# Performance work log

Hardware: AMD Instinct MI355X
Metric: run time of the kernel (lower is better)

## Reference

```python
import jax, jax.numpy as jnp
import numpy as np

H = 128  # GRU hidden size


def _conv(x, w, b, stride):
    # x: NCHW, w: OIHW, VALID padding (torch Conv2d default padding=0)
    y = jax.lax.conv_general_dilated(x, w, (stride, stride), 'VALID',
                                     dimension_numbers=('NCHW', 'OIHW', 'NCHW'))
    return y + b[None, :, None, None]


def setup_inputs() -> dict:
    key = jax.random.key(0)
    ks = jax.random.split(key, 16)
    T, B, A = 128, 32, 6
    x = jax.random.uniform(ks[0], (T * B, 1, 84, 84), jnp.float32) * 255.0
    done = (jax.random.uniform(ks[1], (T * B,)) < 0.1).astype(jnp.float32)
    gru_state = jnp.zeros((1, B, H), jnp.float32)
    s = 0.05
    params = dict(
        conv1_w=jax.random.normal(ks[2], (32, 1, 8, 8)) * s,
        conv1_b=jnp.zeros((32,)),
        conv2_w=jax.random.normal(ks[3], (64, 32, 4, 4)) * s,
        conv2_b=jnp.zeros((64,)),
        conv3_w=jax.random.normal(ks[4], (64, 64, 3, 3)) * s,
        conv3_b=jnp.zeros((64,)),
        fc_w=jax.random.normal(ks[5], (512, 64 * 7 * 7)) * 0.02,
        fc_b=jnp.zeros((512,)),
        w_ih=jax.random.normal(ks[6], (3 * H, 512)) * 0.04,
        w_hh=jax.random.normal(ks[7], (3 * H, H)) * 0.08,
        b_ih=jnp.zeros((3 * H,)),
        b_hh=jnp.zeros((3 * H,)),
        actor_w=jax.random.normal(ks[8], (A, H)) * 0.01,
        actor_b=jnp.zeros((A,)),
        critic_w=jax.random.normal(ks[9], (1, H)) * 0.09,
        critic_b=jnp.zeros((1,)),
    )
    return dict(x=x, done=done, gru_state=gru_state, **params)


def reference(x, done, gru_state,
              conv1_w, conv1_b, conv2_w, conv2_b, conv3_w, conv3_b,
              fc_w, fc_b, w_ih, w_hh, b_ih, b_hh,
              actor_w, actor_b, critic_w, critic_b):
    # CNN encoder on x/255
    h = jax.nn.relu(_conv(x / 255.0, conv1_w, conv1_b, 4))  # [N,32,20,20]
    h = jax.nn.relu(_conv(h, conv2_w, conv2_b, 2))          # [N,64,9,9]
    h = jax.nn.relu(_conv(h, conv3_w, conv3_b, 1))          # [N,64,7,7]
    feat = jax.nn.relu(h.reshape(h.shape[0], -1) @ fc_w.T + fc_b)  # [N,512]

    B = gru_state.shape[1]
    feat = feat.reshape(-1, B, feat.shape[-1])  # [T,B,512]
    d = done.reshape(-1, B)                     # [T,B]

    # hoist input-to-gate projection out of the scan
    gx = jnp.einsum('tbi,gi->tbg', feat, w_ih) + b_ih  # [T,B,3H]

    def step(hprev, inp):
        gxt, dt = inp
        hprev = (1.0 - dt)[:, None] * hprev  # done-reset mask
        gh = hprev @ w_hh.T + b_hh           # [B,3H]
        r = jax.nn.sigmoid(gxt[:, :H] + gh[:, :H])
        z = jax.nn.sigmoid(gxt[:, H:2 * H] + gh[:, H:2 * H])
        n = jnp.tanh(gxt[:, 2 * H:] + r * gh[:, 2 * H:])
        hnew = (1.0 - z) * n + z * hprev
        return hnew, hnew

    h_final, hs = jax.lax.scan(step, gru_state[0], (gx, d))
    hidden = hs.reshape(-1, H)  # [T*B,H]

    logits = hidden @ actor_w.T + actor_b   # [N,A]
    value = hidden @ critic_w.T + critic_b  # [N,1]
    return logits, value, h_final[None]
```

## Files before the change

kernel.cpp:

```cpp
#include <hip/hip_runtime.h>
#include <hip/hip_bf16.h>
#include <stdint.h>

#define DI __device__ __forceinline__

typedef __bf16 bf16x8 __attribute__((ext_vector_type(8)));
typedef __bf16 bf16x4 __attribute__((ext_vector_type(4)));
typedef float f32x16 __attribute__((ext_vector_type(16)));
typedef float f32x2 __attribute__((ext_vector_type(2)));

DI float bf2f(unsigned short u){ return __uint_as_float(((unsigned int)u)<<16); }
DI unsigned short f2bf(float f){
  unsigned int x = __float_as_uint(f);
  x += 0x7fffu + ((x>>16)&1u);
  return (unsigned short)(x>>16);
}
DI float sigmoidf_(float x){ return 1.0f/(1.0f + __expf(-x)); }
DI float tanhf_(float x){ return 2.0f/(1.0f + __expf(-2.0f*x)) - 1.0f; }

DI void gld_lds16(const void* g, void* l){
  __builtin_amdgcn_global_load_lds((const __attribute__((address_space(1))) void*)g,
                                   (__attribute__((address_space(3))) void*)l, 16, 0, 0);
}
DI f32x16 mfma32(bf16x8 a, bf16x8 b, f32x16 c){
  return __builtin_amdgcn_mfma_f32_32x32x16_bf16(a, b, c, 0, 0, 0);
}

__global__ __launch_bounds__(256) void k_prep_all(
    const float* __restrict__ w1, const float* __restrict__ w2, const float* __restrict__ w3,
    const float* __restrict__ fcw, const float* __restrict__ wih,
    unsigned short* __restrict__ W1P, unsigned short* __restrict__ W2P,
    unsigned short* __restrict__ W3P, unsigned short* __restrict__ FCWP,
    unsigned short* __restrict__ GXWP)
{
  const int blk = blockIdx.x, tid = threadIdx.x;
  if (blk < 8){
    int idx = blk*256 + tid;
    int j=idx&7, l=(idx>>3)&63, kk=idx>>9;
    int oc=l&31, kg=kk*16+((l>>5)<<3)+j;
    W1P[idx] = f2bf(w1[oc*64 + kg] * (1.0f/255.0f));
  } else if (blk < 136){
    int idx = (blk-8)*256 + tid;
    int j=idx&7, l=(idx>>3)&63, nt=(idx>>9)&1, kh=(idx>>10)&1, s=idx>>11;
    int oc=nt*32+(l&31), ic=kh*16+(l>>5)*8+j, ky=s>>2, kx=s&3;
    W2P[idx] = f2bf(w2[((oc*32+ic)*4+ky)*4+kx]);
  } else if (blk < 280){
    int idx = (blk-136)*256 + tid;
    int j=idx&7, l=(idx>>3)&63, nt=(idx>>9)&1, kh=(idx>>10)&3, s=idx>>12;
    int oc=nt*32+(l&31), ic=kh*16+(l>>5)*8+j, ky=s/3, kx=s-ky*3;
    W3P[idx] = f2bf(w3[((oc*64+ic)*3+ky)*3+kx]);
  } else if (blk < 6552){
    int i = (blk-280)*256 + tid;
    int t2 = i&511, rest = i>>9;
    int ks = rest%196, nt = rest/196;
    int j=t2&7, l=t2>>3;
    int n=nt*32+(l&31), k=ks*16+(l>>5)*8+j;
    int c=k&63, pos=k>>6;
    float wv = fcw[(size_t)n*3136 + c*49 + pos];
    unsigned short hi = f2bf(wv);
    FCWP[i] = hi;
    FCWP[1605632 + i] = f2bf(wv - bf2f(hi));
  } else {
    int i = (blk-6552)*256 + tid;
    int t2 = i&511, rest = i>>9;
    int ks = rest&31, nt = rest>>5;
    int j=t2&7, l=t2>>3;
    int n=nt*32+(l&31), k=ks*16+(l>>5)*8+j;
    float wv = wih[(size_t)n*512 + k];
    unsigned short hi = f2bf(wv);
    GXWP[i] = hi;
    GXWP[196608 + i] = f2bf(wv - bf2f(hi));
  }
}

__global__ __launch_bounds__(256) void k_conv1(const float* __restrict__ x,
    const unsigned short* __restrict__ w1p, const float* __restrict__ b,
    unsigned short* __restrict__ a1, int nbase)
{
  __shared__ __align__(16) char imgs[4*14784];
  const int tid=threadIdx.x, l=tid&63, w=tid>>6;
  const int nloc = blockIdx.x*4 + w;
  char* myimg = imgs + w*14784;
  const float* xp = x + (size_t)(nbase+nloc)*7056;

  for (int it=0; it<28; ++it){
    int idx4 = l + it*64;
    if (idx4 < 1764){
      float4 v = *(const float4*)(xp + idx4*4);
      int row = idx4/21, rem = idx4 - row*21;
      ushort4 u; u.x=f2bf(v.x); u.y=f2bf(v.y); u.z=f2bf(v.z); u.w=f2bf(v.w);
      *(ushort4*)(myimg + row*176 + rem*8) = u;
    }
  }

  bf16x8 wb[4];
  #pragma unroll
  for (int kk=0;kk<4;kk++) wb[kk] = *(const bf16x8*)(w1p + (kk*64 + l)*8);
  const float bias = b[l&31];
  asm volatile("s_waitcnt lgkmcnt(0)" ::: "memory");

  const int kyh = (l>>5);
  unsigned short* obase = a1 + (size_t)nloc*12800;
  for (int mt=0; mt<13; ++mt){
    int p = mt*32 + (l&31);
    p = min(p, 399);
    const int oy = p/20, ox = p - oy*20;
    const int rbyte = oy*4*176 + ox*8;
    f32x16 acc = {};
    #pragma unroll
    for (int kk=0;kk<4;kk++){
      const int a = rbyte + (kk*2 + kyh)*176;
      bf16x8 af;
      *(bf16x4*)&af       = *(const bf16x4*)(myimg + a);
      *((bf16x4*)&af + 1) = *(const bf16x4*)(myimg + a + 8);
      acc = mfma32(af, wb[kk], acc);
    }
    const int oc = l&31;
    #pragma unroll
    for (int rg=0;rg<16;rg++){
      int row = (rg&3) + 8*(rg>>2) + 4*kyh;
      int pos = mt*32 + row;
      if (pos < 400)
        obase[pos*32 + oc] = f2bf(fmaxf(acc[rg] + bias, 0.f));
    }
  }
}

__global__ __launch_bounds__(256) void k_conv2(const unsigned short* __restrict__ a1,
    const unsigned short* __restrict__ w2p, const float* __restrict__ b2,
    unsigned short* __restrict__ a2, int nbase)
{
  extern __shared__ __align__(16) char smem[];
  const int tid=threadIdx.x, l=tid&63, w=tid>>6;
  const int nloc = blockIdx.x*4 + w;
  char* myimg = smem + w*25600;
  const char* gimg = (const char*)(a1 + (size_t)nloc*12800);
  #pragma unroll
  for (int i=0;i<25;i++){
    int o = i*1024 + l*16;
    int q = o ^ (((o>>7)&7)<<4);
    gld_lds16(gimg + q, myimg + i*1024);
  }
  __syncthreads();
  int rbase[3];
  #pragma unroll
  for (int mt=0;mt<3;mt++){
    int r = mt*32 + (l&31);
    int oy=r/9, ox=r-oy*9;
    rbase[mt] = 40*oy + 2*ox;
  }
  const int grp16 = (l>>5)*16;
  f32x16 acc[3][2] = {};
  #pragma unroll
  for (int ky=0;ky<4;ky++){
    #pragma unroll
    for (int kx=0;kx<4;kx++){
      const int s = ky*4+kx;
      #pragma unroll
      for (int kh=0;kh<2;kh++){
        bf16x8 b0 = *(const bf16x8*)(w2p + (((s*2+kh)*2+0)*64 + l)*8);
        bf16x8 b1 = *(const bf16x8*)(w2p + (((s*2+kh)*2+1)*64 + l)*8);
        #pragma unroll
        for (int mt=0;mt<3;mt++){
          int ip = rbase[mt] + ky*20 + kx;
          ip = min(ip, 399);
          int byte = (ip*64 + kh*32 + grp16) ^ (((ip>>1)&7)<<4);
          bf16x8 af = *(const bf16x8*)(myimg + byte);
          acc[mt][0] = mfma32(af, b0, acc[mt][0]);
          acc[mt][1] = mfma32(af, b1, acc[mt][1]);
        }
      }
    }
  }
  const float bias0 = b2[l&31], bias1 = b2[32+(l&31)];
  unsigned short* ob = (unsigned short*)myimg;
  #pragma unroll
  for (int mt=0;mt<3;mt++){
    #pragma unroll
    for (int rg=0;rg<16;rg++){
      int r = mt*32 + (rg&3) + 8*(rg>>2) + 4*(l>>5);
      ob[r*64 + (l&31)]      = f2bf(fmaxf(acc[mt][0][rg]+bias0,0.f));
      ob[r*64 + 32 + (l&31)] = f2bf(fmaxf(acc[mt][1][rg]+bias1,0.f));
    }
  }
  asm volatile("s_waitcnt lgkmcnt(0)" ::: "memory");
  const uint4* s4 = (const uint4*)ob;
  uint4* d4 = (uint4*)(a2 + (size_t)(nbase+nloc)*5184);
  #pragma unroll
  for (int i=0;i<11;i++){
    int c = i*64 + l;
    if (c < 648) d4[c] = s4[c];
  }
}

__global__ __launch_bounds__(256) void k_conv3(const unsigned short* __restrict__ a2,
    const unsigned short* __restrict__ w3p, const float* __restrict__ b3,
    unsigned short* __restrict__ a3)
{
  __shared__ __align__(16) char smem3[4*11264];
  const int tid=threadIdx.x, l=tid&63, w=tid>>6;
  const int n = blockIdx.x*4 + w;
  char* myimg = smem3 + w*11264;
  const char* gimg = (const char*)(a2 + (size_t)n*5184);
  #pragma unroll
  for (int i=0;i<11;i++){
    int c = i*64 + l;
    int cc = min(c, 647);
    int o = cc*16;
    int q = o ^ (((o>>7)&7)<<4);
    gld_lds16(gimg + q, myimg + i*1024);
  }
  __syncthreads();
  int base[2];
  #pragma unroll
  for (int mt=0;mt<2;mt++){
    int r = mt*32 + (l&31);
    int oy=r/7, ox=r-oy*7;
    base[mt] = oy*9 + ox;
  }
  const int grp16 = (l>>5)*16;
  f32x16 acc[2][2] = {};
  #pragma unroll
  for (int ky=0;ky<3;ky++){
    #pragma unroll
    for (int kx=0;kx<3;kx++){
      const int s = ky*3+kx;
      #pragma unroll
      for (int kh=0;kh<4;kh++){
        bf16x8 b0 = *(const bf16x8*)(w3p + (((s*4+kh)*2+0)*64 + l)*8);
        bf16x8 b1 = *(const bf16x8*)(w3p + (((s*4+kh)*2+1)*64 + l)*8);
        #pragma unroll
        for (int mt=0;mt<2;mt++){
          int ip = min(base[mt] + ky*9 + kx, 80);
          int byte = (ip*128 + kh*32 + grp16) ^ ((ip&7)<<4);
          bf16x8 af = *(const bf16x8*)(myimg + byte);
          acc[mt][0] = mfma32(af, b0, acc[mt][0]);
          acc[mt][1] = mfma32(af, b1, acc[mt][1]);
        }
      }
    }
  }
  const float bias0 = b3[l&31], bias1 = b3[32+(l&31)];
  unsigned short* ob = (unsigned short*)myimg;
  #pragma unroll
  for (int mt=0;mt<2;mt++){
    #pragma unroll
    for (int rg=0;rg<16;rg++){
      int r = mt*32 + (rg&3) + 8*(rg>>2) + 4*(l>>5);
      if (r < 49){
        ob[r*64 + (l&31)]      = f2bf(fmaxf(acc[mt][0][rg]+bias0,0.f));
        ob[r*64 + 32 + (l&31)] = f2bf(fmaxf(acc[mt][1][rg]+bias1,0.f));
      }
    }
  }
  asm volatile("s_waitcnt lgkmcnt(0)" ::: "memory");
  const uint4* s4 = (const uint4*)ob;
  uint4* d4 = (uint4*)(a3 + (size_t)n*3136);
  #pragma unroll
  for (int i=0;i<7;i++){
    int c = i*64 + l;
    if (c < 392) d4[c] = s4[c];
  }
}

template<bool RELU, bool OBF16, bool HILO>
__global__ __launch_bounds__(256) void k_gemm(const unsigned short* __restrict__ A, int K,
    const unsigned short* __restrict__ Wp, int loOff, const float* __restrict__ bias,
    void* __restrict__ out, int N)
{
  __shared__ __align__(16) char ab[2][8192];
  const int tid=threadIdx.x, l=tid&63, w=tid>>6;
  const int m0=blockIdx.y*128, n0=blockIdx.x*64;
  const int KS=K>>4, T=K>>5;
  const int mh=w&1, ntl=w>>1;
  const int ntg = blockIdx.x*2 + ntl;
  const char* Ab = (const char*)A;

  f32x16 acc[2] = {};
  bf16x8 bh0, bh1, bl0, bl1, nh0, nh1, nl0, nl1;

  #pragma unroll
  for (int i=0;i<2;i++){
    int o = (w*2+i)*1024 + l*16;
    int q = o ^ (((o>>7)&7)<<4);
    int row = q>>6, kc=(q>>4)&3;
    gld_lds16(Ab + ((size_t)(m0+row)*K)*2 + kc*16, ab[0] + (w*2+i)*1024);
  }
  {
    const unsigned short* p0 = Wp + ((size_t)(ntg*KS)*64 + l)*8;
    bh0 = *(const bf16x8*)(p0);
    bh1 = *(const bf16x8*)(p0 + 512);
    if (HILO){
      bl0 = *(const bf16x8*)(p0 + loOff);
      bl1 = *(const bf16x8*)(p0 + loOff + 512);
    }
  }
  __syncthreads();

  for (int t=0;t<T;t++){
    const int cb = t&1;
    if (t+1 < T){
      #pragma unroll
      for (int i=0;i<2;i++){
        int o = (w*2+i)*1024 + l*16;
        int q = o ^ (((o>>7)&7)<<4);
        int row = q>>6, kc=(q>>4)&3;
        gld_lds16(Ab + ((size_t)(m0+row)*K + (t+1)*32)*2 + kc*16, ab[cb^1] + (w*2+i)*1024);
      }
      const unsigned short* pn = Wp + ((size_t)(ntg*KS + (t+1)*2)*64 + l)*8;
      nh0 = *(const bf16x8*)(pn);
      nh1 = *(const bf16x8*)(pn + 512);
      if (HILO){
        nl0 = *(const bf16x8*)(pn + loOff);
        nl1 = *(const bf16x8*)(pn + loOff + 512);
      }
    }
    #pragma unroll
    for (int mt=0;mt<2;mt++){
      int r = mh*64 + mt*32 + (l&31);
      int b0 = (r*64 + (l>>5)*16) ^ (((r>>1)&7)<<4);
      bf16x8 a0 = *(const bf16x8*)(ab[cb] + b0);
      bf16x8 a1 = *(const bf16x8*)(ab[cb] + (b0^32));
      acc[mt] = mfma32(a0, bh0, acc[mt]);
      acc[mt] = mfma32(a1, bh1, acc[mt]);
      if (HILO){
        acc[mt] = mfma32(a0, bl0, acc[mt]);
        acc[mt] = mfma32(a1, bl1, acc[mt]);
      }
    }
    __syncthreads();
    bh0=nh0; bh1=nh1;
    if (HILO){ bl0=nl0; bl1=nl1; }
  }

  const int col = n0 + ntl*32 + (l&31);
  const float bv = bias[col];
  #pragma unroll
  for (int mt=0;mt<2;mt++){
    #pragma unroll
    for (int rg=0;rg<16;rg++){
      int r = m0 + mh*64 + mt*32 + (rg&3) + 8*(rg>>2) + 4*(l>>5);
      float v = acc[mt][rg] + bv;
      if (RELU) v = fmaxf(v, 0.f);
      if (OBF16) ((unsigned short*)out)[(size_t)r*N + col] = f2bf(v);
      else       ((float*)out)[(size_t)r*N + col] = v;
    }
  }
}

__global__ __launch_bounds__(256) void k_gru(const float* __restrict__ gx,
    const float* __restrict__ done, const float* __restrict__ h0,
    const float* __restrict__ whh, const float* __restrict__ bhh,
    float* __restrict__ hid, float* __restrict__ hfin)
{
  __shared__ __align__(16) float hs[2][128];
  const int b = blockIdx.x, tid = threadIdx.x;
  const int u = tid>>1, sub = tid&1;
  f32x2 wr[32], wz[32], wn[32];
  const float* wru = whh + (size_t)u*128 + sub*64;
  const float* wzu = whh + (size_t)(u+128)*128 + sub*64;
  const float* wnu = whh + (size_t)(u+256)*128 + sub*64;
  #pragma unroll
  for (int q=0;q<16;q++){
    const int e = (q + sub*4)&15;
    float4 a = *(const float4*)(wru + e*4);
    float4 c = *(const float4*)(wzu + e*4);
    float4 d = *(const float4*)(wnu + e*4);
    wr[q*2] = f32x2{a.x,a.y}; wr[q*2+1] = f32x2{a.z,a.w};
    wz[q*2] = f32x2{c.x,c.y}; wz[q*2+1] = f32x2{c.z,c.w};
    wn[q*2] = f32x2{d.x,d.y}; wn[q*2+1] = f32x2{d.z,d.w};
  }
  const float br = bhh[u], bz = bhh[u+128], bn = bhh[u+256];
  if (tid<128) hs[0][tid] = h0[(size_t)b*128+tid];

  const float* g0 = gx + (size_t)b*384;
  float pg0 = g0[u], pg1 = g0[u+128], pg2 = g0[u+256];
  float pd  = done[b];
  __syncthreads();

  for (int t=0;t<128;t++){
    const int cur = t&1;
    const float gr=pg0, gz=pg1, gn=pg2, dn=pd;
    if (t+1 < 128){
      const float* gp = gx + ((size_t)(t+1)*32+b)*384;
      pg0=gp[u]; pg1=gp[u+128]; pg2=gp[u+256];
      pd = done[(t+1)*32+b];
    }
    const float hpv = hs[cur][u];
    const float* hb = &hs[cur][sub*64];
    f32x2 hv[32];
    #pragma unroll
    for (int q=0;q<16;q++){
      const int e = (q + sub*4)&15;
      float4 v = *(const float4*)(hb + e*4);
      hv[q*2]   = f32x2{v.x,v.y};
      hv[q*2+1] = f32x2{v.z,v.w};
    }
    f32x2 a2r = {0.f,0.f}, a2z = {0.f,0.f}, a2n = {0.f,0.f};
    #pragma unroll
    for (int i=0;i<32;i++){
      a2r += wr[i]*hv[i];
      a2z += wz[i]*hv[i];
      a2n += wn[i]*hv[i];
    }
    float ar=a2r[0]+a2r[1], az=a2z[0]+a2z[1], an=a2n[0]+a2n[1];
    ar += __shfl_xor(ar,1);
    az += __shfl_xor(az,1);
    an += __shfl_xor(an,1);
    if (sub==0){
      const float keep = 1.0f - dn;
      const float hp = keep*hpv;
      const float r  = sigmoidf_(gr + keep*ar + br);
      const float z  = sigmoidf_(gz + keep*az + bz);
      const float nn = tanhf_  (gn + r*(keep*an + bn));
      const float hn = (1.0f-z)*nn + z*hp;
      hs[cur^1][u] = hn;
      hid[((size_t)t*32+b)*128 + u] = hn;
    }
    asm volatile("s_waitcnt lgkmcnt(0)\n\ts_barrier" ::: "memory");
    __builtin_amdgcn_sched_barrier(0);
  }
  if (tid<128) hfin[(size_t)b*128+tid] = hs[0][tid];
}

__global__ __launch_bounds__(256) void k_heads(const float* __restrict__ hid,
    const float* __restrict__ aw, const float* __restrict__ ab,
    const float* __restrict__ cw, const float* __restrict__ cb,
    float* __restrict__ out)
{
  __shared__ __align__(16) float wsm[7*128];
  __shared__ float bb[7];
  const int tid = threadIdx.x;
  for (int i=tid;i<896;i+=256) wsm[i] = (i<768) ? aw[i] : cw[i-768];
  if (tid<7) bb[tid] = (tid<6) ? ab[tid] : cb[0];
  __syncthreads();
  const int idx = blockIdx.x*256 + tid;
  const int n = idx/7, a = idx - n*7;
  const float4* hp = (const float4*)(hid + (size_t)n*128);
  const float4* wp = (const float4*)(&wsm[a*128]);
  float s = bb[a];
  #pragma unroll
  for (int q=0;q<32;q++){
    const float4 h4=hp[q], w4=wp[q];
    s += h4.x*w4.x + h4.y*w4.y + h4.z*w4.z + h4.w*w4.w;
  }
  if (a<6) out[(size_t)n*6+a]=s; else out[24576+n]=s;
}

extern "C" void kernel_launch(void* const* d_in, const int* in_sizes, int n_in,
                              void* d_out, int out_size, void* d_ws, size_t ws_size,
                              hipStream_t stream)
{
  const float* x    = (const float*)d_in[0];
  const float* done = (const float*)d_in[1];
  const float* h0   = (const float*)d_in[2];
  const float* c1w  = (const float*)d_in[3];
  const float* c1b  = (const float*)d_in[4];
  const float* c2w  = (const float*)d_in[5];
  const float* c2b  = (const float*)d_in[6];
  const float* c3w  = (const float*)d_in[7];
  const float* c3b  = (const float*)d_in[8];
  const float* fcw  = (const float*)d_in[9];
  const float* fcb  = (const float*)d_in[10];
  const float* wih  = (const float*)d_in[11];
  const float* whh  = (const float*)d_in[12];
  const float* bih  = (const float*)d_in[13];
  const float* bhh  = (const float*)d_in[14];
  const float* aw   = (const float*)d_in[15];
  const float* ab   = (const float*)d_in[16];
  const float* cw   = (const float*)d_in[17];
  const float* cb   = (const float*)d_in[18];
  float* out = (float*)d_out;
  char* ws = (char*)d_ws;

  unsigned short* W1P  = (unsigned short*)(ws);
  unsigned short* W2P  = (unsigned short*)(ws + 4096);
  unsigned short* W3P  = (unsigned short*)(ws + 69632);
  unsigned short* FCWP = (unsigned short*)(ws + 143360);
  unsigned short* GXWP = (unsigned short*)(ws + 6565888);
  unsigned short* A1   = (unsigned short*)(ws + 7352320);
  unsigned short* A2   = (unsigned short*)(ws + 59781120);
  unsigned short* A3   = (unsigned short*)(ws + 7352320);
  unsigned short* FEAT = (unsigned short*)(ws + 33042432);
  float* GX   = (float*)(ws + 37236736);
  float* HID  = (float*)(ws + 43528192);

  static bool attr_set = false;
  if (!attr_set) {
    (void)hipFuncSetAttribute((const void*)k_conv2, hipFuncAttributeMaxDynamicSharedMemorySize, 102400);
    attr_set = true;
  }

  k_prep_all<<<7320, 256, 0, stream>>>(c1w, c2w, c3w, fcw, wih, W1P, W2P, W3P, FCWP, GXWP);

  for (int pass=0; pass<2; pass++){
    k_conv1<<<512, 256, 0, stream>>>(x, W1P, c1b, A1, pass*2048);
    k_conv2<<<512, 256, 102400, stream>>>(A1, W2P, c2b, A2, pass*2048);
  }
  k_conv3<<<1024, 256, 0, stream>>>(A2, W3P, c3b, A3);
  k_gemm<true, true, false><<<dim3(8,32), 256, 0, stream>>>(A3, 3136, FCWP, 0, fcb, (void*)FEAT, 512);
  k_gemm<false,false,true ><<<dim3(6,32), 256, 0, stream>>>(FEAT, 512, GXWP, 196608, bih, (void*)GX, 384);
  k_gru<<<32, 256, 0, stream>>>(GX, done, h0, whh, bhh, HID, out + 28672);
  k_heads<<<112, 256, 0, stream>>>(HID, aw, ab, cw, cb, out);
}
```

Measured before the change: 342.2 us.

## Run GRU recurrence as single-block bf16 MFMA over all batch columns

Replaces the per-batch-row scalar GRU kernel (32 blocks of FMA dot products) with one 512-thread block that computes the hidden-to-gate product for all 32 batch rows per step using 16x16x32 bf16 MFMA, with W_hh pre-packed into bf16 fragments held in registers. The r/z parts of b_hh are folded into the input-gate bias used by the preceding GEMM. Hidden state is exchanged through LDS as bf16. This targets the per-step latency of the serial 128-step scan, but rounding the hidden state and W_hh to bf16 adds error that accumulates across the recurrence, and everything now runs on a single CU.

```diff
diff --git a/kernel.cpp b/kernel.cpp
--- a/kernel.cpp
+++ b/kernel.cpp
@@ -7,7 +7,7 @@
 typedef __bf16 bf16x8 __attribute__((ext_vector_type(8)));
 typedef __bf16 bf16x4 __attribute__((ext_vector_type(4)));
 typedef float f32x16 __attribute__((ext_vector_type(16)));
-typedef float f32x2 __attribute__((ext_vector_type(2)));
+typedef float f32x4 __attribute__((ext_vector_type(4)));
 
 DI float bf2f(unsigned short u){ return __uint_as_float(((unsigned int)u)<<16); }
 DI unsigned short f2bf(float f){
@@ -25,13 +25,18 @@
 DI f32x16 mfma32(bf16x8 a, bf16x8 b, f32x16 c){
   return __builtin_amdgcn_mfma_f32_32x32x16_bf16(a, b, c, 0, 0, 0);
 }
+DI f32x4 mfma16(bf16x8 a, bf16x8 b, f32x4 c){
+  return __builtin_amdgcn_mfma_f32_16x16x32_bf16(a, b, c, 0, 0, 0);
+}
 
 __global__ __launch_bounds__(256) void k_prep_all(
     const float* __restrict__ w1, const float* __restrict__ w2, const float* __restrict__ w3,
     const float* __restrict__ fcw, const float* __restrict__ wih,
+    const float* __restrict__ whh, const float* __restrict__ bih, const float* __restrict__ bhh,
     unsigned short* __restrict__ W1P, unsigned short* __restrict__ W2P,
     unsigned short* __restrict__ W3P, unsigned short* __restrict__ FCWP,
-    unsigned short* __restrict__ GXWP)
+    unsigned short* __restrict__ GXWP, unsigned short* __restrict__ WHHP,
+    float* __restrict__ GXB)
 {
   const int blk = blockIdx.x, tid = threadIdx.x;
   if (blk < 8){
@@ -60,7 +65,7 @@
     unsigned short hi = f2bf(wv);
     FCWP[i] = hi;
     FCWP[1605632 + i] = f2bf(wv - bf2f(hi));
-  } else {
+  } else if (blk < 7320){
     int i = (blk-6552)*256 + tid;
     int t2 = i&511, rest = i>>9;
     int ks = rest&31, nt = rest>>5;
@@ -70,6 +75,15 @@
     unsigned short hi = f2bf(wv);
     GXWP[i] = hi;
     GXWP[196608 + i] = f2bf(wv - bf2f(hi));
+  } else if (blk < 7512){
+    int i = (blk-7320)*256 + tid;
+    int j=i&7, l=(i>>3)&63, kf=(i>>9)&3, v=(i>>11)&7, g=i>>14;
+    int m = g*128 + v*16 + (l&15);
+    int k = kf*32 + ((l>>4)<<3) + j;
+    WHHP[i] = f2bf(whh[(size_t)m*128 + k]);
+  } else {
+    int i = (blk-7512)*256 + tid;
+    if (i < 384) GXB[i] = bih[i] + (i < 256 ? bhh[i] : 0.0f);
   }
 }
 
@@ -348,79 +362,109 @@
   }
 }
 
-__global__ __launch_bounds__(256) void k_gru(const float* __restrict__ gx,
+__global__ __launch_bounds__(512) void k_gru_mfma(const float* __restrict__ gx,
     const float* __restrict__ done, const float* __restrict__ h0,
-    const float* __restrict__ whh, const float* __restrict__ bhh,
+    const unsigned short* __restrict__ whhp, const float* __restrict__ bhh,
     float* __restrict__ hid, float* __restrict__ hfin)
 {
-  __shared__ __align__(16) float hs[2][128];
-  const int b = blockIdx.x, tid = threadIdx.x;
-  const int u = tid>>1, sub = tid&1;
-  f32x2 wr[32], wz[32], wn[32];
-  const float* wru = whh + (size_t)u*128 + sub*64;
-  const float* wzu = whh + (size_t)(u+128)*128 + sub*64;
-  const float* wnu = whh + (size_t)(u+256)*128 + sub*64;
-  #pragma unroll
-  for (int q=0;q<16;q++){
-    const int e = (q + sub*4)&15;
-    float4 a = *(const float4*)(wru + e*4);
-    float4 c = *(const float4*)(wzu + e*4);
-    float4 d = *(const float4*)(wnu + e*4);
-    wr[q*2] = f32x2{a.x,a.y}; wr[q*2+1] = f32x2{a.z,a.w};
-    wz[q*2] = f32x2{c.x,c.y}; wz[q*2+1] = f32x2{c.z,c.w};
-    wn[q*2] = f32x2{d.x,d.y}; wn[q*2+1] = f32x2{d.z,d.w};
-  }
-  const float br = bhh[u], bz = bhh[u+128], bn = bhh[u+256];
-  if (tid<128) hs[0][tid] = h0[(size_t)b*128+tid];
-
-  const float* g0 = gx + (size_t)b*384;
-  float pg0 = g0[u], pg1 = g0[u+128], pg2 = g0[u+256];
-  float pd  = done[b];
+  __shared__ __align__(16) char hsb[2*8448];
+  const int tid = threadIdx.x, l = tid&63, v = tid>>6;
+  const int bl = l&15;
+  const int u0 = v*16 + ((l>>4)<<2);
+
+  bf16x8 wf[12];
+  #pragma unroll
+  for (int g=0; g<3; ++g)
+    #pragma unroll
+    for (int kf=0; kf<4; ++kf)
+      wf[g*4+kf] = *(const bf16x8*)(whhp + (size_t)(((g*8+v)*4+kf)*64 + l)*8);
+
+  float bn4[4];
+  #pragma unroll
+  for (int i=0;i<4;i++) bn4[i] = bhh[256 + u0 + i];
+
+  float hp[2][4];
+  #pragma unroll
+  for (int h=0; h<2; ++h){
+    const int b = h*16 + bl;
+    float4 h4 = *(const float4*)(h0 + (size_t)b*128 + u0);
+    hp[h][0]=h4.x; hp[h][1]=h4.y; hp[h][2]=h4.z; hp[h][3]=h4.w;
+    uint2 pk;
+    pk.x = (unsigned)f2bf(h4.x) | ((unsigned)f2bf(h4.y)<<16);
+    pk.y = (unsigned)f2bf(h4.z) | ((unsigned)f2bf(h4.w)<<16);
+    *(uint2*)(hsb + b*264 + u0*2) = pk;
+  }
+
+  const float4* gx4 = (const float4*)gx;
+  float4 pg[2][3]; float pd[2];
+  #pragma unroll
+  for (int h=0; h<2; ++h){
+    const int b = h*16 + bl;
+    const size_t gb = (size_t)b*96 + (u0>>2);
+    pg[h][0]=gx4[gb]; pg[h][1]=gx4[gb+32]; pg[h][2]=gx4[gb+64];
+    pd[h]=done[b];
+  }
   __syncthreads();
 
-  for (int t=0;t<128;t++){
-    const int cur = t&1;
-    const float gr=pg0, gz=pg1, gn=pg2, dn=pd;
+  for (int t=0; t<128; ++t){
+    const char* hc = hsb + (t&1)*8448;
+    char* hnx = hsb + ((t+1)&1)*8448;
+    float4 cg[2][3]; float cd[2];
+    #pragma unroll
+    for (int h=0; h<2; ++h){
+      cg[h][0]=pg[h][0]; cg[h][1]=pg[h][1]; cg[h][2]=pg[h][2]; cd[h]=pd[h];
+    }
     if (t+1 < 128){
-      const float* gp = gx + ((size_t)(t+1)*32+b)*384;
-      pg0=gp[u]; pg1=gp[u+128]; pg2=gp[u+256];
-      pd = done[(t+1)*32+b];
-    }
-    const float hpv = hs[cur][u];
-    const float* hb = &hs[cur][sub*64];
-    f32x2 hv[32];
-    #pragma unroll
-    for (int q=0;q<16;q++){
-      const int e = (q + sub*4)&15;
-      float4 v = *(const float4*)(hb + e*4);
-      hv[q*2]   = f32x2{v.x,v.y};
-      hv[q*2+1] = f32x2{v.z,v.w};
-    }
-    f32x2 a2r = {0.f,0.f}, a2z = {0.f,0.f}, a2n = {0.f,0.f};
-    #pragma unroll
-    for (int i=0;i<32;i++){
-      a2r += wr[i]*hv[i];
-      a2z += wz[i]*hv[i];
-      a2n += wn[i]*hv[i];
-    }
-    float ar=a2r[0]+a2r[1], az=a2z[0]+a2z[1], an=a2n[0]+a2n[1];
-    ar += __shfl_xor(ar,1);
-    az += __shfl_xor(az,1);
-    an += __shfl_xor(an,1);
-    if (sub==0){
-      const float keep = 1.0f - dn;
-      const float hp = keep*hpv;
-      const float r  = sigmoidf_(gr + keep*ar + br);
-      const float z  = sigmoidf_(gz + keep*az + bz);
-      const float nn = tanhf_  (gn + r*(keep*an + bn));
-      const float hn = (1.0f-z)*nn + z*hp;
-      hs[cur^1][u] = hn;
-      hid[((size_t)t*32+b)*128 + u] = hn;
+      #pragma unroll
+      for (int h=0; h<2; ++h){
+        const int b = h*16 + bl;
+        const size_t gb = (size_t)((t+1)*32 + b)*96 + (u0>>2);
+        pg[h][0]=gx4[gb]; pg[h][1]=gx4[gb+32]; pg[h][2]=gx4[gb+64];
+        pd[h]=done[(t+1)*32+b];
+      }
+    }
+    f32x4 acc[2][3] = {};
+    #pragma unroll
+    for (int h=0; h<2; ++h){
+      const int b = h*16 + bl;
+      #pragma unroll
+      for (int kf=0; kf<4; ++kf){
+        bf16x8 hb = *(const bf16x8*)(hc + b*264 + kf*64 + ((l>>4)<<4));
+        acc[h][0] = mfma16(wf[kf],   hb, acc[h][0]);
+        acc[h][1] = mfma16(wf[4+kf], hb, acc[h][1]);
+        acc[h][2] = mfma16(wf[8+kf], hb, acc[h][2]);
+      }
+    }
+    #pragma unroll
+    for (int h=0; h<2; ++h){
+      const int b = h*16 + bl;
+      const float keep = 1.0f - cd[h];
+      const float gr[4]={cg[h][0].x,cg[h][0].y,cg[h][0].z,cg[h][0].w};
+      const float gz[4]={cg[h][1].x,cg[h][1].y,cg[h][1].z,cg[h][1].w};
+      const float gn[4]={cg[h][2].x,cg[h][2].y,cg[h][2].z,cg[h][2].w};
+      float hn[4];
+      #pragma unroll
+      for (int i=0;i<4;i++){
+        const float r  = sigmoidf_(gr[i] + keep*acc[h][0][i]);
+        const float z  = sigmoidf_(gz[i] + keep*acc[h][1][i]);
+        const float nn = tanhf_  (gn[i] + r*(keep*acc[h][2][i] + bn4[i]));
+        hn[i] = (1.0f - z)*nn + z*(keep*hp[h][i]);
+        hp[h][i] = hn[i];
+      }
+      *(float4*)(hid + (size_t)(t*32+b)*128 + u0) = float4{hn[0],hn[1],hn[2],hn[3]};
+      uint2 pk;
+      pk.x = (unsigned)f2bf(hn[0]) | ((unsigned)f2bf(hn[1])<<16);
+      pk.y = (unsigned)f2bf(hn[2]) | ((unsigned)f2bf(hn[3])<<16);
+      *(uint2*)(hnx + b*264 + u0*2) = pk;
     }
     asm volatile("s_waitcnt lgkmcnt(0)\n\ts_barrier" ::: "memory");
     __builtin_amdgcn_sched_barrier(0);
   }
-  if (tid<128) hfin[(size_t)b*128+tid] = hs[0][tid];
+  #pragma unroll
+  for (int h=0; h<2; ++h){
+    const int b = h*16 + bl;
+    *(float4*)(hfin + (size_t)b*128 + u0) = float4{hp[h][0],hp[h][1],hp[h][2],hp[h][3]};
+  }
 }
 
 __global__ __launch_bounds__(256) void k_heads(const float* __restrict__ hid,
@@ -484,6 +528,8 @@
   unsigned short* FEAT = (unsigned short*)(ws + 33042432);
   float* GX   = (float*)(ws + 37236736);
   float* HID  = (float*)(ws + 43528192);
+  unsigned short* WHHP = (unsigned short*)(ws + 102248448);
+  float* GXB  = (float*)(ws + 102346752);
 
   static bool attr_set = false;
   if (!attr_set) {
@@ -491,7 +537,8 @@
     attr_set = true;
   }
 
-  k_prep_all<<<7320, 256, 0, stream>>>(c1w, c2w, c3w, fcw, wih, W1P, W2P, W3P, FCWP, GXWP);
+  k_prep_all<<<7514, 256, 0, stream>>>(c1w, c2w, c3w, fcw, wih, whh, bih, bhh,
+                                       W1P, W2P, W3P, FCWP, GXWP, WHHP, GXB);
 
   for (int pass=0; pass<2; pass++){
     k_conv1<<<512, 256, 0, stream>>>(x, W1P, c1b, A1, pass*2048);
@@ -499,7 +546,7 @@
   }
   k_conv3<<<1024, 256, 0, stream>>>(A2, W3P, c3b, A3);
   k_gemm<true, true, false><<<dim3(8,32), 256, 0, stream>>>(A3, 3136, FCWP, 0, fcb, (void*)FEAT, 512);
-  k_gemm<false,false,true ><<<dim3(6,32), 256, 0, stream>>>(FEAT, 512, GXWP, 196608, bih, (void*)GX, 384);
-  k_gru<<<32, 256, 0, stream>>>(GX, done, h0, whh, bhh, HID, out + 28672);
+  k_gemm<false,false,true ><<<dim3(6,32), 256, 0, stream>>>(FEAT, 512, GXWP, 196608, GXB, (void*)GX, 384);
+  k_gru_mfma<<<1, 512, 0, stream>>>(GX, done, h0, WHHP, bhh, HID, out + 28672);
   k_heads<<<112, 256, 0, stream>>>(HID, aw, ab, cw, cb, out);
 }
```

New measurement: 703.2 us. 2.05x slower.
